# Kernel tuning notes

Hardware: AMD Instinct MI355X
Metric: run time of the kernel (lower is better)

## Reference

```python
import jax, jax.numpy as jnp
import numpy as np

INPUT_DIM = 128
HIDDEN = 64
HEAD_DIM = 16
NUM_HEADS = 32
BATCH = 131072


def _xavier(key, shape, fan_in, fan_out):
    limit = np.sqrt(6.0 / (fan_in + fan_out))
    return jax.random.uniform(key, shape, jnp.float32, -limit, limit)


def setup_inputs() -> dict:
    key = jax.random.key(0)
    ks = jax.random.split(key, 6)
    x = jax.random.normal(ks[0], (BATCH, INPUT_DIM), jnp.float32)
    # backbone: Linear(input,hidden)+ReLU, Linear(hidden,hidden)+ReLU
    W0 = _xavier(ks[1], (INPUT_DIM, HIDDEN), INPUT_DIM, HIDDEN)
    b0 = jnp.zeros((HIDDEN,), jnp.float32)
    W1 = _xavier(ks[2], (HIDDEN, HIDDEN), HIDDEN, HIDDEN)
    b1 = jnp.zeros((HIDDEN,), jnp.float32)
    # heads (xavier on flattened [num_heads, -1] view, matching torch init)
    hw1 = _xavier(ks[3], (NUM_HEADS, HIDDEN, HEAD_DIM), NUM_HEADS, HIDDEN * HEAD_DIM)
    hb1 = jnp.zeros((NUM_HEADS, HEAD_DIM), jnp.float32)
    hw2 = _xavier(ks[4], (NUM_HEADS, HEAD_DIM, 1), NUM_HEADS, HEAD_DIM)
    hb2 = jnp.zeros((NUM_HEADS, 1), jnp.float32)
    return {"x": x, "W0": W0, "b0": b0, "W1": W1, "b1": b1,
            "heads_w1": hw1, "heads_b1": hb1, "heads_w2": hw2, "heads_b2": hb2}


def reference(x, W0, b0, W1, b1, heads_w1, heads_b1, heads_w2, heads_b2):
    # shared backbone: two Linear+ReLU layers
    f = jax.nn.relu(x @ W0 + b0)            # [B, hidden]
    f = jax.nn.relu(f @ W1 + b1)            # [B, hidden]
    # parallel heads
    h = jnp.einsum('bh,nhd->bnd', f, heads_w1) + heads_b1  # [B, N, D]
    h = jax.nn.relu(h)
    logits = jnp.einsum('bnd,ndo->bno', h, heads_w2) + heads_b2  # [B, N, 1]
    return logits[..., 0]                   # [B, N]
```

## Files before the change

kernel.cpp:

```cpp
#include <hip/hip_runtime.h>
#include <stdint.h>

typedef __attribute__((ext_vector_type(8))) short short8;
typedef __attribute__((ext_vector_type(4))) float f32x4;

#define B_TOTAL     131072
#define WG_THREADS  512
#define WAVES       8
#define T_TILES     1
#define ROWS_PER_WG (WAVES * T_TILES * 16)
#define NUM_WG      (B_TOTAL / ROWS_PER_WG)

#define A1_SH   0
#define A2_SH   8192
#define A3_SH   12288
#define W2V_OFF 90112

#define FSTRIDE 72
#define SMEM_SHORTS (WAVES * 16 * FSTRIDE)
#define OSTRIDE 33

__device__ __forceinline__ short f2bf(float x) {
  union { float f; uint32_t u; } v; v.f = x;
  uint32_t r = (v.u + 0x7FFFu + ((v.u >> 16) & 1u)) >> 16;
  return (short)r;
}

__device__ __forceinline__ uint32_t pack2(float a, float b) {
  return (uint32_t)(uint16_t)f2bf(a) | ((uint32_t)(uint16_t)f2bf(b) << 16);
}

__global__ void prep_kernel(const float* __restrict__ W0, const float* __restrict__ W1,
                            const float* __restrict__ hw1, const float* __restrict__ hw2,
                            short* __restrict__ wsA, float* __restrict__ w2v) {
  int idx = blockIdx.x * 256 + threadIdx.x;
  int stride = gridDim.x * 256;
  for (int i = idx; i < 8192; i += stride) {
    int j = i & 7, l = (i >> 3) & 63, kt = (i >> 9) & 3, mt = i >> 11;
    int m = mt * 16 + (l & 15), k = kt * 32 + (l >> 4) * 8 + j;
    wsA[A1_SH + i] = f2bf(W0[k * 64 + m]);
  }
  for (int i = idx; i < 4096; i += stride) {
    int j = i & 7, l = (i >> 3) & 63, kt = (i >> 9) & 1, mt = i >> 10;
    int m = mt * 16 + (l & 15), k = kt * 32 + (l >> 4) * 8 + j;
    wsA[A2_SH + i] = f2bf(W1[k * 64 + m]);
  }
  for (int i = idx; i < 32768; i += stride) {
    int j = i & 7, l = (i >> 3) & 63, kt = (i >> 9) & 1, n = i >> 10;
    int d = l & 15, k = kt * 32 + (l >> 4) * 8 + j;
    wsA[A3_SH + i] = f2bf(hw1[(n * 64 + k) * 16 + d]);
  }
  for (int i = idx; i < 8192; i += stride) {
    int ii = i & 3, l = (i >> 2) & 63, n = i >> 8;
    w2v[i] = hw2[n * 16 + (l >> 4) * 4 + ii];
  }
}

__global__ __launch_bounds__(WG_THREADS, 4)
void mhc_kernel(const float* __restrict__ x, const float* __restrict__ b0,
                const float* __restrict__ b1, const float* __restrict__ hb1,
                const float* __restrict__ hb2, const short* __restrict__ wsA,
                const float* __restrict__ w2v, float* __restrict__ out) {
  __shared__ short smem[SMEM_SHORTS];
  __shared__ float obuf[WAVES * 16 * OSTRIDE];

  const int tid = threadIdx.x;
  const int w = tid >> 6, l = tid & 63;
  const int g = l >> 4, c = l & 15;
  const int rowbase = blockIdx.x * ROWS_PER_WG + w * (T_TILES * 16);

  short* fw = smem + w * (16 * FSTRIDE);
  float* ow = obuf + w * (16 * OSTRIDE);

  for (int t = 0; t < T_TILES; ++t) {
    const float* xp = x + (size_t)(rowbase + t * 16 + c) * 128 + g * 8;
    float4 xr[4][2];
#pragma unroll
    for (int kt = 0; kt < 4; ++kt) {
      xr[kt][0] = *(const float4*)(xp + kt * 32);
      xr[kt][1] = *(const float4*)(xp + kt * 32 + 4);
    }
    short8 bx[4];
#pragma unroll
    for (int kt = 0; kt < 4; ++kt) {
      float4 a = xr[kt][0], bq = xr[kt][1];
      short8 v;
      v[0] = f2bf(a.x);  v[1] = f2bf(a.y);  v[2] = f2bf(a.z);  v[3] = f2bf(a.w);
      v[4] = f2bf(bq.x); v[5] = f2bf(bq.y); v[6] = f2bf(bq.z); v[7] = f2bf(bq.w);
      bx[kt] = v;
    }
#pragma unroll
    for (int mt = 0; mt < 4; ++mt) {
      f32x4 acc = {0.f, 0.f, 0.f, 0.f};
#pragma unroll
      for (int kt = 0; kt < 4; ++kt)
        acc = __builtin_amdgcn_mfma_f32_16x16x32_bf16(
            *(const short8*)(wsA + A1_SH + ((mt * 4 + kt) * 64 + l) * 8),
            bx[kt], acc, 0, 0, 0);
      float4 bv = *(const float4*)(b0 + mt * 16 + g * 4);
      uint2 pp;
      pp.x = pack2(fmaxf(acc[0] + bv.x, 0.f), fmaxf(acc[1] + bv.y, 0.f));
      pp.y = pack2(fmaxf(acc[2] + bv.z, 0.f), fmaxf(acc[3] + bv.w, 0.f));
      *(uint2*)(fw + c * FSTRIDE + mt * 16 + g * 4) = pp;
    }
    short8 b2_0 = *(const short8*)(fw + c * FSTRIDE + g * 8);
    short8 b2_1 = *(const short8*)(fw + c * FSTRIDE + 32 + g * 8);
#pragma unroll
    for (int mt = 0; mt < 4; ++mt) {
      f32x4 acc = {0.f, 0.f, 0.f, 0.f};
      acc = __builtin_amdgcn_mfma_f32_16x16x32_bf16(
          *(const short8*)(wsA + A2_SH + ((mt * 2 + 0) * 64 + l) * 8), b2_0, acc, 0, 0, 0);
      acc = __builtin_amdgcn_mfma_f32_16x16x32_bf16(
          *(const short8*)(wsA + A2_SH + ((mt * 2 + 1) * 64 + l) * 8), b2_1, acc, 0, 0, 0);
      float4 bv = *(const float4*)(b1 + mt * 16 + g * 4);
      uint2 pp;
      pp.x = pack2(fmaxf(acc[0] + bv.x, 0.f), fmaxf(acc[1] + bv.y, 0.f));
      pp.y = pack2(fmaxf(acc[2] + bv.z, 0.f), fmaxf(acc[3] + bv.w, 0.f));
      *(uint2*)(fw + c * FSTRIDE + mt * 16 + g * 4) = pp;
    }
    short8 b3_0 = *(const short8*)(fw + c * FSTRIDE + g * 8);
    short8 b3_1 = *(const short8*)(fw + c * FSTRIDE + 32 + g * 8);

#pragma unroll 2
    for (int n = 0; n < 32; ++n) {
      short8 a30 = *(const short8*)(wsA + A3_SH + ((n * 2 + 0) * 64 + l) * 8);
      short8 a31 = *(const short8*)(wsA + A3_SH + ((n * 2 + 1) * 64 + l) * 8);
      float4 wl  = *(const float4*)(w2v + n * 256 + l * 4);
      float4 hbv = *(const float4*)(hb1 + n * 16 + g * 4);
      f32x4 acc = {0.f, 0.f, 0.f, 0.f};
      acc = __builtin_amdgcn_mfma_f32_16x16x32_bf16(a30, b3_0, acc, 0, 0, 0);
      acc = __builtin_amdgcn_mfma_f32_16x16x32_bf16(a31, b3_1, acc, 0, 0, 0);
      float s = fmaxf(acc[0] + hbv.x, 0.f) * wl.x
              + fmaxf(acc[1] + hbv.y, 0.f) * wl.y
              + fmaxf(acc[2] + hbv.z, 0.f) * wl.z
              + fmaxf(acc[3] + hbv.w, 0.f) * wl.w;
      s += __shfl_xor(s, 16);
      s += __shfl_xor(s, 32);
      s += hb2[n];
      if (g == (n >> 3)) ow[c * OSTRIDE + n] = s;
    }
    float r[8];
#pragma unroll
    for (int j = 0; j < 8; ++j) r[j] = ow[c * OSTRIDE + g * 8 + j];
    float4 v0 = {r[0], r[1], r[2], r[3]};
    float4 v1 = {r[4], r[5], r[6], r[7]};
    float* op = out + (size_t)(rowbase + t * 16 + c) * 32 + g * 8;
    *(float4*)op = v0;
    *(float4*)(op + 4) = v1;
  }
}

extern "C" void kernel_launch(void* const* d_in, const int* in_sizes, int n_in,
                              void* d_out, int out_size, void* d_ws, size_t ws_size,
                              hipStream_t stream) {
  const float* x   = (const float*)d_in[0];
  const float* W0  = (const float*)d_in[1];
  const float* b0  = (const float*)d_in[2];
  const float* W1  = (const float*)d_in[3];
  const float* b1  = (const float*)d_in[4];
  const float* hw1 = (const float*)d_in[5];
  const float* hb1 = (const float*)d_in[6];
  const float* hw2 = (const float*)d_in[7];
  const float* hb2 = (const float*)d_in[8];
  float* out = (float*)d_out;

  short* wsA = (short*)d_ws;
  float* w2v = (float*)((char*)d_ws + W2V_OFF);

  prep_kernel<<<128, 256, 0, stream>>>(W0, W1, hw1, hw2, wsA, w2v);
  mhc_kernel<<<NUM_WG, WG_THREADS, 0, stream>>>(x, b0, b1, hb1, hb2, wsA, w2v, out);
}
```

Measured before the change: 159.4 us.

## Stage head weights in LDS and process four row tiles per wave with paired head MFMAs

Each workgroup now copies the 64 KB head-layer weight block from global memory into shared memory once, then each wave processes 64 rows (four 16-row tiles, handled in pairs). The head loop reuses each A-fragment across two row tiles, and the second-layer head weights are read straight from hw2 instead of a prepacked buffer. The aim is to cut repeated global/L2 fetches of the head weights and amortize the weight loads. In exchange it uses about 64 KB of LDS per workgroup, which may limit occupancy, and launches a quarter as many workgroups.

```diff
diff --git a/kernel.cpp b/kernel.cpp
--- a/kernel.cpp
+++ b/kernel.cpp
@@ -7,17 +7,14 @@
 #define B_TOTAL     131072
 #define WG_THREADS  512
 #define WAVES       8
-#define T_TILES     1
-#define ROWS_PER_WG (WAVES * T_TILES * 16)
+#define ROWS_PER_WG (WAVES * 4 * 16)
 #define NUM_WG      (B_TOTAL / ROWS_PER_WG)
 
 #define A1_SH   0
 #define A2_SH   8192
 #define A3_SH   12288
-#define W2V_OFF 90112
 
 #define FSTRIDE 72
-#define SMEM_SHORTS (WAVES * 16 * FSTRIDE)
 #define OSTRIDE 33
 
 __device__ __forceinline__ short f2bf(float x) {
@@ -31,8 +28,7 @@
 }
 
 __global__ void prep_kernel(const float* __restrict__ W0, const float* __restrict__ W1,
-                            const float* __restrict__ hw1, const float* __restrict__ hw2,
-                            short* __restrict__ wsA, float* __restrict__ w2v) {
+                            const float* __restrict__ hw1, short* __restrict__ wsA) {
   int idx = blockIdx.x * 256 + threadIdx.x;
   int stride = gridDim.x * 256;
   for (int i = idx; i < 8192; i += stride) {
@@ -50,103 +46,132 @@
     int d = l & 15, k = kt * 32 + (l >> 4) * 8 + j;
     wsA[A3_SH + i] = f2bf(hw1[(n * 64 + k) * 16 + d]);
   }
-  for (int i = idx; i < 8192; i += stride) {
-    int ii = i & 3, l = (i >> 2) & 63, n = i >> 8;
-    w2v[i] = hw2[n * 16 + (l >> 4) * 4 + ii];
-  }
 }
 
 __global__ __launch_bounds__(WG_THREADS, 4)
 void mhc_kernel(const float* __restrict__ x, const float* __restrict__ b0,
                 const float* __restrict__ b1, const float* __restrict__ hb1,
-                const float* __restrict__ hb2, const short* __restrict__ wsA,
-                const float* __restrict__ w2v, float* __restrict__ out) {
-  __shared__ short smem[SMEM_SHORTS];
-  __shared__ float obuf[WAVES * 16 * OSTRIDE];
+                const float* __restrict__ hb2, const float* __restrict__ hw2,
+                const short* __restrict__ wsA, float* __restrict__ out) {
+  __shared__ short a3s[32768];
+  __shared__ short fwbuf[WAVES * 16 * FSTRIDE];
+  __shared__ float obuf[WAVES * 2 * 16 * OSTRIDE];
 
   const int tid = threadIdx.x;
   const int w = tid >> 6, l = tid & 63;
   const int g = l >> 4, c = l & 15;
-  const int rowbase = blockIdx.x * ROWS_PER_WG + w * (T_TILES * 16);
+  const int rowbase = blockIdx.x * ROWS_PER_WG + w * 64;
 
-  short* fw = smem + w * (16 * FSTRIDE);
-  float* ow = obuf + w * (16 * OSTRIDE);
+  {
+    const uint4* src = (const uint4*)(wsA + A3_SH);
+    uint4* dst = (uint4*)a3s;
+    for (int i = tid; i < 4096; i += WG_THREADS) dst[i] = src[i];
+  }
+  __syncthreads();
 
-  for (int t = 0; t < T_TILES; ++t) {
-    const float* xp = x + (size_t)(rowbase + t * 16 + c) * 128 + g * 8;
-    float4 xr[4][2];
+  short* fw = fwbuf + w * (16 * FSTRIDE);
+  float* ow = obuf + w * (2 * 16 * OSTRIDE);
+
+  for (int tp = 0; tp < 2; ++tp) {
+    const int trow = rowbase + tp * 32;
+
+    float4 xr[2][4][2];
 #pragma unroll
-    for (int kt = 0; kt < 4; ++kt) {
-      xr[kt][0] = *(const float4*)(xp + kt * 32);
-      xr[kt][1] = *(const float4*)(xp + kt * 32 + 4);
+    for (int tt = 0; tt < 2; ++tt) {
+      const float* xp = x + (size_t)(trow + tt * 16 + c) * 128 + g * 8;
+#pragma unroll
+      for (int kt = 0; kt < 4; ++kt) {
+        xr[tt][kt][0] = *(const float4*)(xp + kt * 32);
+        xr[tt][kt][1] = *(const float4*)(xp + kt * 32 + 4);
+      }
     }
-    short8 bx[4];
+
+    short8 b3[2][2];
 #pragma unroll
-    for (int kt = 0; kt < 4; ++kt) {
-      float4 a = xr[kt][0], bq = xr[kt][1];
-      short8 v;
-      v[0] = f2bf(a.x);  v[1] = f2bf(a.y);  v[2] = f2bf(a.z);  v[3] = f2bf(a.w);
-      v[4] = f2bf(bq.x); v[5] = f2bf(bq.y); v[6] = f2bf(bq.z); v[7] = f2bf(bq.w);
-      bx[kt] = v;
+    for (int tt = 0; tt < 2; ++tt) {
+      short8 bx[4];
+#pragma unroll
+      for (int kt = 0; kt < 4; ++kt) {
+        float4 a = xr[tt][kt][0], bq = xr[tt][kt][1];
+        short8 v;
+        v[0] = f2bf(a.x);  v[1] = f2bf(a.y);  v[2] = f2bf(a.z);  v[3] = f2bf(a.w);
+        v[4] = f2bf(bq.x); v[5] = f2bf(bq.y); v[6] = f2bf(bq.z); v[7] = f2bf(bq.w);
+        bx[kt] = v;
+      }
+#pragma unroll
+      for (int mt = 0; mt < 4; ++mt) {
+        f32x4 acc = {0.f, 0.f, 0.f, 0.f};
+#pragma unroll
+        for (int kt = 0; kt < 4; ++kt)
+          acc = __builtin_amdgcn_mfma_f32_16x16x32_bf16(
+              *(const short8*)(wsA + A1_SH + ((mt * 4 + kt) * 64 + l) * 8),
+              bx[kt], acc, 0, 0, 0);
+        float4 bv = *(const float4*)(b0 + mt * 16 + g * 4);
+        uint2 pp;
+        pp.x = pack2(fmaxf(acc[0] + bv.x, 0.f), fmaxf(acc[1] + bv.y, 0.f));
+        pp.y = pack2(fmaxf(acc[2] + bv.z, 0.f), fmaxf(acc[3] + bv.w, 0.f));
+        *(uint2*)(fw + c * FSTRIDE + mt * 16 + g * 4) = pp;
+      }
+      short8 b2_0 = *(const short8*)(fw + c * FSTRIDE + g * 8);
+      short8 b2_1 = *(const short8*)(fw + c * FSTRIDE + 32 + g * 8);
+#pragma unroll
+      for (int mt = 0; mt < 4; ++mt) {
+        f32x4 acc = {0.f, 0.f, 0.f, 0.f};
+        acc = __builtin_amdgcn_mfma_f32_16x16x32_bf16(
+            *(const short8*)(wsA + A2_SH + ((mt * 2 + 0) * 64 + l) * 8), b2_0, acc, 0, 0, 0);
+        acc = __builtin_amdgcn_mfma_f32_16x16x32_bf16(
+            *(const short8*)(wsA + A2_SH + ((mt * 2 + 1) * 64 + l) * 8), b2_1, acc, 0, 0, 0);
+        float4 bv = *(const float4*)(b1 + mt * 16 + g * 4);
+        uint2 pp;
+        pp.x = pack2(fmaxf(acc[0] + bv.x, 0.f), fmaxf(acc[1] + bv.y, 0.f));
+        pp.y = pack2(fmaxf(acc[2] + bv.z, 0.f), fmaxf(acc[3] + bv.w, 0.f));
+        *(uint2*)(fw + c * FSTRIDE + mt * 16 + g * 4) = pp;
+      }
+      b3[tt][0] = *(const short8*)(fw + c * FSTRIDE + g * 8);
+      b3[tt][1] = *(const short8*)(fw + c * FSTRIDE + 32 + g * 8);
     }
-#pragma unroll
-    for (int mt = 0; mt < 4; ++mt) {
-      f32x4 acc = {0.f, 0.f, 0.f, 0.f};
-#pragma unroll
-      for (int kt = 0; kt < 4; ++kt)
-        acc = __builtin_amdgcn_mfma_f32_16x16x32_bf16(
-            *(const short8*)(wsA + A1_SH + ((mt * 4 + kt) * 64 + l) * 8),
-            bx[kt], acc, 0, 0, 0);
-      float4 bv = *(const float4*)(b0 + mt * 16 + g * 4);
-      uint2 pp;
-      pp.x = pack2(fmaxf(acc[0] + bv.x, 0.f), fmaxf(acc[1] + bv.y, 0.f));
-      pp.y = pack2(fmaxf(acc[2] + bv.z, 0.f), fmaxf(acc[3] + bv.w, 0.f));
-      *(uint2*)(fw + c * FSTRIDE + mt * 16 + g * 4) = pp;
-    }
-    short8 b2_0 = *(const short8*)(fw + c * FSTRIDE + g * 8);
-    short8 b2_1 = *(const short8*)(fw + c * FSTRIDE + 32 + g * 8);
-#pragma unroll
-    for (int mt = 0; mt < 4; ++mt) {
-      f32x4 acc = {0.f, 0.f, 0.f, 0.f};
-      acc = __builtin_amdgcn_mfma_f32_16x16x32_bf16(
-          *(const short8*)(wsA + A2_SH + ((mt * 2 + 0) * 64 + l) * 8), b2_0, acc, 0, 0, 0);
-      acc = __builtin_amdgcn_mfma_f32_16x16x32_bf16(
-          *(const short8*)(wsA + A2_SH + ((mt * 2 + 1) * 64 + l) * 8), b2_1, acc, 0, 0, 0);
-      float4 bv = *(const float4*)(b1 + mt * 16 + g * 4);
-      uint2 pp;
-      pp.x = pack2(fmaxf(acc[0] + bv.x, 0.f), fmaxf(acc[1] + bv.y, 0.f));
-      pp.y = pack2(fmaxf(acc[2] + bv.z, 0.f), fmaxf(acc[3] + bv.w, 0.f));
-      *(uint2*)(fw + c * FSTRIDE + mt * 16 + g * 4) = pp;
-    }
-    short8 b3_0 = *(const short8*)(fw + c * FSTRIDE + g * 8);
-    short8 b3_1 = *(const short8*)(fw + c * FSTRIDE + 32 + g * 8);
 
 #pragma unroll 2
     for (int n = 0; n < 32; ++n) {
-      short8 a30 = *(const short8*)(wsA + A3_SH + ((n * 2 + 0) * 64 + l) * 8);
-      short8 a31 = *(const short8*)(wsA + A3_SH + ((n * 2 + 1) * 64 + l) * 8);
-      float4 wl  = *(const float4*)(w2v + n * 256 + l * 4);
+      short8 a30 = *(const short8*)(a3s + (n * 2 + 0) * 512 + l * 8);
+      short8 a31 = *(const short8*)(a3s + (n * 2 + 1) * 512 + l * 8);
+      float4 wl  = *(const float4*)(hw2 + n * 16 + g * 4);
       float4 hbv = *(const float4*)(hb1 + n * 16 + g * 4);
-      f32x4 acc = {0.f, 0.f, 0.f, 0.f};
-      acc = __builtin_amdgcn_mfma_f32_16x16x32_bf16(a30, b3_0, acc, 0, 0, 0);
-      acc = __builtin_amdgcn_mfma_f32_16x16x32_bf16(a31, b3_1, acc, 0, 0, 0);
-      float s = fmaxf(acc[0] + hbv.x, 0.f) * wl.x
-              + fmaxf(acc[1] + hbv.y, 0.f) * wl.y
-              + fmaxf(acc[2] + hbv.z, 0.f) * wl.z
-              + fmaxf(acc[3] + hbv.w, 0.f) * wl.w;
-      s += __shfl_xor(s, 16);
-      s += __shfl_xor(s, 32);
-      s += hb2[n];
-      if (g == (n >> 3)) ow[c * OSTRIDE + n] = s;
+      float hb2n = hb2[n];
+      f32x4 acc0 = {0.f, 0.f, 0.f, 0.f};
+      f32x4 acc1 = {0.f, 0.f, 0.f, 0.f};
+      acc0 = __builtin_amdgcn_mfma_f32_16x16x32_bf16(a30, b3[0][0], acc0, 0, 0, 0);
+      acc1 = __builtin_amdgcn_mfma_f32_16x16x32_bf16(a30, b3[1][0], acc1, 0, 0, 0);
+      acc0 = __builtin_amdgcn_mfma_f32_16x16x32_bf16(a31, b3[0][1], acc0, 0, 0, 0);
+      acc1 = __builtin_amdgcn_mfma_f32_16x16x32_bf16(a31, b3[1][1], acc1, 0, 0, 0);
+      float s0 = fmaxf(acc0[0] + hbv.x, 0.f) * wl.x
+               + fmaxf(acc0[1] + hbv.y, 0.f) * wl.y
+               + fmaxf(acc0[2] + hbv.z, 0.f) * wl.z
+               + fmaxf(acc0[3] + hbv.w, 0.f) * wl.w;
+      float s1 = fmaxf(acc1[0] + hbv.x, 0.f) * wl.x
+               + fmaxf(acc1[1] + hbv.y, 0.f) * wl.y
+               + fmaxf(acc1[2] + hbv.z, 0.f) * wl.z
+               + fmaxf(acc1[3] + hbv.w, 0.f) * wl.w;
+      s0 += __shfl_xor(s0, 16);  s1 += __shfl_xor(s1, 16);
+      s0 += __shfl_xor(s0, 32);  s1 += __shfl_xor(s1, 32);
+      s0 += hb2n;                s1 += hb2n;
+      if (g == (n >> 3)) {
+        ow[c * OSTRIDE + n] = s0;
+        ow[16 * OSTRIDE + c * OSTRIDE + n] = s1;
+      }
     }
-    float r[8];
+
 #pragma unroll
-    for (int j = 0; j < 8; ++j) r[j] = ow[c * OSTRIDE + g * 8 + j];
-    float4 v0 = {r[0], r[1], r[2], r[3]};
-    float4 v1 = {r[4], r[5], r[6], r[7]};
-    float* op = out + (size_t)(rowbase + t * 16 + c) * 32 + g * 8;
-    *(float4*)op = v0;
-    *(float4*)(op + 4) = v1;
+    for (int tt = 0; tt < 2; ++tt) {
+      float r[8];
+#pragma unroll
+      for (int j = 0; j < 8; ++j) r[j] = ow[tt * 16 * OSTRIDE + c * OSTRIDE + g * 8 + j];
+      float4 v0 = {r[0], r[1], r[2], r[3]};
+      float4 v1 = {r[4], r[5], r[6], r[7]};
+      float* op = out + (size_t)(trow + tt * 16 + c) * 32 + g * 8;
+      *(float4*)op = v0;
+      *(float4*)(op + 4) = v1;
+    }
   }
 }
 
@@ -165,8 +190,7 @@
   float* out = (float*)d_out;
 
   short* wsA = (short*)d_ws;
-  float* w2v = (float*)((char*)d_ws + W2V_OFF);
 
-  prep_kernel<<<128, 256, 0, stream>>>(W0, W1, hw1, hw2, wsA, w2v);
-  mhc_kernel<<<NUM_WG, WG_THREADS, 0, stream>>>(x, b0, b1, hb1, hb2, wsA, w2v, out);
+  prep_kernel<<<128, 256, 0, stream>>>(W0, W1, hw1, wsA);
+  mhc_kernel<<<NUM_WG, WG_THREADS, 0, stream>>>(x, b0, b1, hb1, hb2, hw2, wsA, out);
 }
```

New measurement: 138.2 us. -13.3%, faster.
